# Kernel tuning notes

Hardware: AMD Instinct MI355X
Metric: run time of the kernel (lower is better)

Reference implementation:

```python
import jax, jax.numpy as jnp
import numpy as np

KD = 3  # kernel size per spatial dim
K = KD * KD * KD  # 27 taps


def conv3d(x, w, b, padding=1):
    # x: [B, C, D, H, W], w: [O, C, kd, kh, kw]
    pad = ((padding, padding),) * 3
    y = jax.lax.conv_general_dilated(
        x, w, window_strides=(1, 1, 1), padding=pad,
        dimension_numbers=('NCDHW', 'OIDHW', 'NCDHW'))
    return y + b[None, :, None, None, None]


def add_coords(x):
    # CoordConv: append 3 normalized coordinate channels in [-1, 1].
    B, C, D, H, W = x.shape
    z = jnp.linspace(-1.0, 1.0, D, dtype=x.dtype)[:, None, None]
    y = jnp.linspace(-1.0, 1.0, H, dtype=x.dtype)[None, :, None]
    xx = jnp.linspace(-1.0, 1.0, W, dtype=x.dtype)[None, None, :]
    coords = jnp.stack([
        jnp.broadcast_to(z, (D, H, W)),
        jnp.broadcast_to(y, (D, H, W)),
        jnp.broadcast_to(xx, (D, H, W)),
    ], axis=0)  # [3, D, H, W]
    coords = jnp.broadcast_to(coords[None], (B, 3, D, H, W))
    return jnp.concatenate([x, coords], axis=1)


def trilinear_sample(x, pos):
    # x: [B, C, D, H, W]; pos: [B, K, 3, D, H, W] absolute (z, y, x) sample coords.
    # Zero padding outside the volume. Returns [B, C, K, D, H, W].
    B, C, D, H, W = x.shape
    Kt = pos.shape[1]
    pz, py, px = pos[:, :, 0], pos[:, :, 1], pos[:, :, 2]  # [B, K, D, H, W]
    fz, fy, fx = jnp.floor(pz), jnp.floor(py), jnp.floor(px)
    x_flat = x.reshape(B, C, D * H * W)
    out = jnp.zeros((B, C, Kt, D, H, W), dtype=x.dtype)
    for cz in (0.0, 1.0):
        for cy in (0.0, 1.0):
            for cx in (0.0, 1.0):
                iz, iy, ix = fz + cz, fy + cy, fx + cx
                wgt = ((1.0 - jnp.abs(pz - iz)) *
                       (1.0 - jnp.abs(py - iy)) *
                       (1.0 - jnp.abs(px - ix)))
                valid = ((iz >= 0) & (iz < D) & (iy >= 0) & (iy < H)
                         & (ix >= 0) & (ix < W))
                izc = jnp.clip(iz, 0, D - 1).astype(jnp.int32)
                iyc = jnp.clip(iy, 0, H - 1).astype(jnp.int32)
                ixc = jnp.clip(ix, 0, W - 1).astype(jnp.int32)
                flat = ((izc * H + iyc) * W + ixc).reshape(B, -1)  # [B, K*DHW]
                vals = jax.vmap(lambda xf, idx: jnp.take(xf, idx, axis=1))(x_flat, flat)
                vals = vals.reshape(B, C, Kt, D, H, W)
                out = out + (wgt * valid.astype(x.dtype))[:, None] * vals
    return out


def modulated_deform_conv3d(x, offsets, alpha, w, b):
    # x: [B, Cin, D, H, W]; offsets: [B, 3K, D, H, W]; alpha: [B, K, D, H, W]
    # w: [O, Cin, 3, 3, 3]; stride 1, padding 1, dilation 1.
    B, Cin, D, H, W = x.shape
    off = offsets.reshape(B, K, 3, D, H, W)
    # Base sampling grid per tap: voxel position + kernel offset (pad=1 -> -1..1).
    dz = jnp.arange(D, dtype=x.dtype)[:, None, None]
    dy = jnp.arange(H, dtype=x.dtype)[None, :, None]
    dx = jnp.arange(W, dtype=x.dtype)[None, None, :]
    base = jnp.stack([
        jnp.broadcast_to(dz, (D, H, W)),
        jnp.broadcast_to(dy, (D, H, W)),
        jnp.broadcast_to(dx, (D, H, W)),
    ], axis=0)  # [3, D, H, W]
    kg = jnp.arange(KD, dtype=x.dtype) - 1.0  # [-1, 0, 1]
    kpos = jnp.stack(jnp.meshgrid(kg, kg, kg, indexing='ij'),
                     axis=-1).reshape(K, 3)  # [K, 3] in (kd, kh, kw) order
    pos = base[None, None] + kpos[None, :, :, None, None, None] + off  # [B,K,3,D,H,W]
    sampled = trilinear_sample(x, pos)  # [B, Cin, K, D, H, W]
    sampled = sampled * alpha[:, None]  # modulation
    wk = w.reshape(w.shape[0], Cin, K)
    out = jnp.einsum('bckv,ock->bov', sampled.reshape(B, Cin, K, D * H * W), wk)
    return out.reshape(B, -1, D, H, W) + b[None, :, None, None, None]


def setup_inputs() -> dict:
    key = jax.random.key(0)
    ks = jax.random.split(key, 4)
    B, Cin, Cout, D, H, W = 2, 64, 64, 8, 32, 32
    x = jax.random.normal(ks[0], (B, Cin, D, H, W), dtype=jnp.float32)
    # Small init on offset branch keeps sampling near the regular grid.
    w_off = jax.random.normal(ks[1], (108, Cin + 3, 3, 3, 3), jnp.float32) * 0.01
    b_off = jnp.zeros((108,), jnp.float32)
    w_dcn = jax.random.normal(ks[2], (Cout, Cin, 3, 3, 3), jnp.float32) * (1.0 / np.sqrt(Cin * 27))
    b_dcn = jnp.zeros((Cout,), jnp.float32)
    return {"x": x, "w_off": w_off, "b_off": b_off, "w_dcn": w_dcn, "b_dcn": b_dcn}


def reference(x, w_off, b_off, w_dcn, b_dcn):
    # CoordConv3d offset/mask prediction
    pred = conv3d(add_coords(x), w_off, b_off, padding=1)  # [B, 108, D, H, W]
    offsets, alpha = pred[:, :81], pred[:, 81:]
    alpha = jax.nn.sigmoid(alpha)  # [B, 27, D, H, W]
    return modulated_deform_conv3d(x, offsets, alpha, w_dcn, b_dcn)
```

## Files before the change

### kernel.cpp

```cpp
#include <hip/hip_runtime.h>

#define DHW  8192
#define COFF 108

typedef __attribute__((ext_vector_type(8))) short bf16x8;
typedef __attribute__((ext_vector_type(4))) float f32x4;
typedef __bf16 bfv2 __attribute__((ext_vector_type(2)));

__device__ inline unsigned short f2bf(float f) {
    unsigned u = __float_as_uint(f);
    u += 0x7fffu + ((u >> 16) & 1u);
    return (unsigned short)(u >> 16);
}
__device__ inline float bf2f(unsigned short h) {
    return __uint_as_float(((unsigned)h) << 16);
}

__device__ inline float dot2bf(unsigned a, unsigned b, float c) {
#if defined(__has_builtin) && __has_builtin(__builtin_amdgcn_fdot2_f32_bf16)
    return __builtin_amdgcn_fdot2_f32_bf16(__builtin_bit_cast(bfv2, a),
                                           __builtin_bit_cast(bfv2, b), c, false);
#else
    c += __uint_as_float(a << 16) * __uint_as_float(b << 16);
    c += __uint_as_float(a & 0xffff0000u) * __uint_as_float(b & 0xffff0000u);
    return c;
#endif
}

__global__ __launch_bounds__(256) void k_prep(
    const float* __restrict__ x, const float* __restrict__ w_off,
    const float* __restrict__ w_dcn,
    ushort* __restrict__ xt, ushort* __restrict__ pA1,
    ushort* __restrict__ pAc, ushort* __restrict__ pW)
{
    __shared__ ushort tile[16 * 66];
    const int bi = blockIdx.x;
    const int tid = threadIdx.x;
    if (bi < 1024) {
        const int b  = bi >> 9;
        const int f0 = (bi & 511) * 16;
        #pragma unroll
        for (int it = 0; it < 4; ++it) {
            int c = it * 16 + (tid >> 4), f = tid & 15;
            tile[f * 66 + c] = f2bf(x[((size_t)(b * 64 + c)) * DHW + f0 + f]);
        }
        __syncthreads();
        #pragma unroll
        for (int it = 0; it < 4; ++it) {
            int f = it * 4 + (tid >> 6), c = tid & 63;
            xt[((size_t)b * DHW + f0 + f) * 64 + c] = tile[f * 66 + c];
        }
    } else {
        int t0 = (bi - 1024) * 256 + tid;
        const int stride = 32 * 256;
        for (int i = t0; i < 27 * 2 * 7 * 512; i += stride) {
            int j = i & 7, l = (i >> 3) & 63, rest = i >> 9;
            int m = rest % 7, ch = (rest / 7) & 1, tap = rest / 14;
            int co = m * 16 + (l & 15);
            int ci = ch * 32 + (l >> 4) * 8 + j;
            pA1[i] = (co < COFF) ? f2bf(w_off[(co * 67 + ci) * 27 + tap]) : (ushort)0;
        }
        for (int i = t0; i < 3 * 7 * 512; i += stride) {
            int j = i & 7, l = (i >> 3) & 63, rest = i >> 9;
            int m = rest % 7, t = rest / 7;
            int co = m * 16 + (l & 15);
            int flatk = t * 32 + (l >> 4) * 8 + j;
            ushort v = 0;
            if (co < COFF && flatk < 81) {
                int cc = flatk / 27, tap = flatk % 27;
                v = f2bf(w_off[(co * 67 + 64 + cc) * 27 + tap]);
            }
            pAc[i] = v;
        }
        for (int i = t0; i < 27 * 2 * 4 * 512; i += stride) {
            int j = i & 7, l = (i >> 3) & 63;
            int m = (i >> 9) & 3, ch = (i >> 11) & 1, k = i >> 12;
            int o = m * 16 + (l & 15);
            int c = ch * 32 + (l >> 4) * 8 + j;
            pW[i] = f2bf(w_dcn[(o * 64 + c) * 27 + k]);
        }
    }
}

__global__ __launch_bounds__(512, 4) void k_fused(
    const ushort* __restrict__ xt, const ushort* __restrict__ pA1,
    const ushort* __restrict__ pAc, const ushort* __restrict__ pW,
    const float* __restrict__ b_off, const float* __restrict__ b_dcn,
    float* __restrict__ out)
{
    __shared__ __align__(16) char smem[64768];
    ushort* pred_lds = (ushort*)smem;
    char*   region   = smem + 6912;

    const int bi   = blockIdx.x;
    const int b    = bi >> 8;
    const int sp32 = bi & 255;
    const int d    = sp32 >> 5;
    const int h    = sp32 & 31;
    const int spg  = sp32 * 32;
    const int tid  = threadIdx.x;
    const int wv = tid >> 6, lane = tid & 63, q = lane >> 4, r16 = lane & 15;
    const ushort* __restrict__ xb = xt + (size_t)b * DHW * 64;

    f32x4 acc1[14] = {};
    for (int c = wv; c < 57; c += 8) {
        bf16x8 bf[2];
        const ushort* pa;
        if (c < 54) {
            int tap = c >> 1, ch = c & 1;
            int dz = tap / 9, rem9 = tap - dz * 9, dy = rem9 / 3, dx = rem9 - dy * 3;
            int zz = d + dz - 1, yy = h + dy - 1;
            int basepos = (zz << 10) + (yy << 5);
            bool okzy = ((unsigned)zz < 8u) & ((unsigned)yy < 32u);
            #pragma unroll
            for (int pt = 0; pt < 2; ++pt) {
                int xx = pt * 16 + r16 + dx - 1;
                bool ok = okzy & ((unsigned)xx < 32u);
                bf16x8 tv = {};
                if (ok) tv = *(const bf16x8*)(xb + (size_t)(basepos + xx) * 64
                                              + ch * 32 + q * 8);
                bf[pt] = tv;
            }
            pa = pA1 + (size_t)((tap * 2 + ch) * 7) * 512 + lane * 8;
        } else {
            int t = c - 54;
            #pragma unroll
            for (int pt = 0; pt < 2; ++pt) {
                bf16x8 bt;
                #pragma unroll
                for (int j = 0; j < 8; ++j) {
                    int flatk = t * 32 + q * 8 + j;
                    int cc = flatk / 27, tap = flatk % 27;
                    int dz = tap / 9, rem9 = tap - dz * 9, dy = rem9 / 3, dx = rem9 - dy * 3;
                    int zz = d + dz - 1, yy = h + dy - 1, xx = pt * 16 + r16 + dx - 1;
                    bool ok = (flatk < 81) & ((unsigned)zz < 8u) & ((unsigned)yy < 32u)
                              & ((unsigned)xx < 32u);
                    float val = 0.f;
                    if (ok)
                        val = (cc == 0) ? (-1.f + (2.f / 7.f) * (float)zz)
                            : (cc == 1) ? (-1.f + (2.f / 31.f) * (float)yy)
                                        : (-1.f + (2.f / 31.f) * (float)xx);
                    bt[j] = (short)f2bf(val);
                }
                bf[pt] = bt;
            }
            pa = pAc + (size_t)(t * 7) * 512 + lane * 8;
        }
        #pragma unroll
        for (int m = 0; m < 7; ++m) {
            bf16x8 af = *(const bf16x8*)(pa + m * 512);
            acc1[m * 2 + 0] = __builtin_amdgcn_mfma_f32_16x16x32_bf16(af, bf[0], acc1[m * 2 + 0], 0, 0, 0);
            acc1[m * 2 + 1] = __builtin_amdgcn_mfma_f32_16x16x32_bf16(af, bf[1], acc1[m * 2 + 1], 0, 0, 0);
        }
    }
    {
        uint2* red1 = (uint2*)region;
        #pragma unroll
        for (int i = 0; i < 14; ++i) {
            f32x4 s = acc1[i];
            uint2 pk2;
            pk2.x = (unsigned)f2bf(s[0]) | ((unsigned)f2bf(s[1]) << 16);
            pk2.y = (unsigned)f2bf(s[2]) | ((unsigned)f2bf(s[3]) << 16);
            red1[(wv * 14 + i) * 64 + lane] = pk2;
        }
        __syncthreads();
        for (int i = wv; i < 14; i += 8) {
            float s0 = 0.f, s1 = 0.f, s2 = 0.f, s3 = 0.f;
            #pragma unroll
            for (int sw = 0; sw < 8; ++sw) {
                uint2 v = red1[(sw * 14 + i) * 64 + lane];
                s0 += bf2f((unsigned short)(v.x & 0xffffu));
                s1 += bf2f((unsigned short)(v.x >> 16));
                s2 += bf2f((unsigned short)(v.y & 0xffffu));
                s3 += bf2f((unsigned short)(v.y >> 16));
            }
            int m = i >> 1, pt = i & 1;
            float sr[4] = {s0, s1, s2, s3};
            #pragma unroll
            for (int r = 0; r < 4; ++r) {
                int co = m * 16 + q * 4 + r;
                if (co < COFF)
                    pred_lds[co * 32 + pt * 16 + r16] = f2bf(sr[r] + b_off[co]);
            }
        }
        __syncthreads();
    }

    uint4* cwi = (uint4*)region;
    uint4* cww = (uint4*)(region + 27648);
    for (int kp = tid; kp < 27 * 32; kp += 512) {
        int k = kp >> 5, p = kp & 31;
        float offz = bf2f(pred_lds[(k * 3 + 0) * 32 + p]);
        float offy = bf2f(pred_lds[(k * 3 + 1) * 32 + p]);
        float offx = bf2f(pred_lds[(k * 3 + 2) * 32 + p]);
        float av   = bf2f(pred_lds[(81 + k) * 32 + p]);
        float alpha = 1.f / (1.f + __expf(-av));
        int kz = k / 9, rem = k - kz * 9, ky = rem / 3, kx = rem - ky * 3;
        float pz = (float)(d + kz - 1) + offz;
        float py = (float)(h + ky - 1) + offy;
        float px = (float)(p + kx - 1) + offx;
        float fz = floorf(pz), fy = floorf(py), fx = floorf(px);
        float tz = pz - fz, ty = py - fy, tx = px - fx;
        int iz0 = (int)fz, iy0 = (int)fy, ix0 = (int)fx;
        unsigned idxs[8]; float wgts[8];
        #pragma unroll
        for (int c8 = 0; c8 < 8; ++c8) {
            int czi = c8 >> 2, cyi = (c8 >> 1) & 1, cxi = c8 & 1;
            int iz = iz0 + czi, iy = iy0 + cyi, ix = ix0 + cxi;
            float wz = czi ? tz : 1.f - tz;
            float wy = cyi ? ty : 1.f - ty;
            float wx = cxi ? tx : 1.f - tx;
            bool ok = ((unsigned)iz < 8u) && ((unsigned)iy < 32u) && ((unsigned)ix < 32u);
            idxs[c8] = ok ? ((unsigned)((iz << 10) + (iy << 5) + ix) << 7) : 0u;
            wgts[c8] = ok ? wz * wy * wx * alpha : 0.f;
        }
        cwi[(k * 2 + 0) * 32 + p] = make_uint4(idxs[0], idxs[1], idxs[2], idxs[3]);
        cwi[(k * 2 + 1) * 32 + p] = make_uint4(idxs[4], idxs[5], idxs[6], idxs[7]);
        cww[k * 32 + p] = make_uint4(
            (unsigned)f2bf(wgts[0]) | ((unsigned)f2bf(wgts[1]) << 16),
            (unsigned)f2bf(wgts[2]) | ((unsigned)f2bf(wgts[3]) << 16),
            (unsigned)f2bf(wgts[4]) | ((unsigned)f2bf(wgts[5]) << 16),
            (unsigned)f2bf(wgts[6]) | ((unsigned)f2bf(wgts[7]) << 16));
    }
    __syncthreads();

    char* Sbuf = region + 41472;
    const int str = wv >> 2, pq = wv & 3;
    const int pr = lane >> 3, cg = lane & 7;
    const int p2 = pq * 8 + pr;
    const int m4 = wv & 3, ch = wv >> 2;
    const char* xbB = (const char*)xb + cg * 16;
    const unsigned swz_w = (unsigned)(str * 8192 + p2 * 128 + ((cg * 16) ^ ((p2 & 7) << 4)));
    unsigned swz_r[2];
    #pragma unroll
    for (int pt = 0; pt < 2; ++pt) {
        int p = pt * 16 + r16;
        swz_r[pt] = (unsigned)(p * 128 + ((ch * 64 + q * 16) ^ ((p & 7) << 4)));
    }

    f32x4 acc2[2] = {};
    for (int t = 0; t < 14; ++t) {
        const int ks0 = 2 * t + str;
        if (ks0 < 27) {
            uint4 wq = cww[ks0 * 32 + p2];
            uint4 i0 = cwi[(ks0 * 2 + 0) * 32 + p2];
            uint4 i1 = cwi[(ks0 * 2 + 1) * 32 + p2];
            unsigned iv[8] = {i0.x, i0.y, i0.z, i0.w, i1.x, i1.y, i1.z, i1.w};
            uint4 xv[8];
            #pragma unroll
            for (int c8 = 0; c8 < 8; ++c8)
                xv[c8] = *(const uint4*)(xbB + iv[c8]);
            unsigned wp[4] = {wq.x, wq.y, wq.z, wq.w};
            float sa[8] = {};
            #pragma unroll
            for (int cp = 0; cp < 4; ++cp) {
                unsigned ua[4] = {xv[cp * 2 + 0].x, xv[cp * 2 + 0].y, xv[cp * 2 + 0].z, xv[cp * 2 + 0].w};
                unsigned ub[4] = {xv[cp * 2 + 1].x, xv[cp * 2 + 1].y, xv[cp * 2 + 1].z, xv[cp * 2 + 1].w};
                #pragma unroll
                for (int dw = 0; dw < 4; ++dw) {
                    unsigned plo = __builtin_amdgcn_perm(ub[dw], ua[dw], 0x05040100u);
                    unsigned phi = __builtin_amdgcn_perm(ub[dw], ua[dw], 0x07060302u);
                    sa[dw * 2 + 0] = dot2bf(plo, wp[cp], sa[dw * 2 + 0]);
                    sa[dw * 2 + 1] = dot2bf(phi, wp[cp], sa[dw * 2 + 1]);
                }
            }
            uint4 pk;
            pk.x = (unsigned)f2bf(sa[0]) | ((unsigned)f2bf(sa[1]) << 16);
            pk.y = (unsigned)f2bf(sa[2]) | ((unsigned)f2bf(sa[3]) << 16);
            pk.z = (unsigned)f2bf(sa[4]) | ((unsigned)f2bf(sa[5]) << 16);
            pk.w = (unsigned)f2bf(sa[6]) | ((unsigned)f2bf(sa[7]) << 16);
            *(uint4*)(Sbuf + (t & 1) * 4096 + swz_w) = pk;
        }
        __syncthreads();
        #pragma unroll
        for (int ks = 0; ks < 2; ++ks) {
            int k = 2 * t + ks;
            if (k < 27) {
                bf16x8 af = *(const bf16x8*)(pW + (size_t)((k * 2 + ch) * 4 + m4) * 512 + lane * 8);
                #pragma unroll
                for (int pt = 0; pt < 2; ++pt) {
                    bf16x8 bv = *(const bf16x8*)(Sbuf + ks * 8192 + (t & 1) * 4096 + swz_r[pt]);
                    acc2[pt] = __builtin_amdgcn_mfma_f32_16x16x32_bf16(af, bv, acc2[pt], 0, 0, 0);
                }
            }
        }
    }

    __syncthreads();
    f32x4* red2 = (f32x4*)(region + 41472);
    if (wv >= 4) {
        red2[(m4 * 2 + 0) * 64 + lane] = acc2[0];
        red2[(m4 * 2 + 1) * 64 + lane] = acc2[1];
    }
    __syncthreads();
    if (wv < 4) {
        float* __restrict__ outb = out + (size_t)b * 64 * DHW + spg;
        #pragma unroll
        for (int pt = 0; pt < 2; ++pt) {
            f32x4 s = acc2[pt] + red2[(m4 * 2 + pt) * 64 + lane];
            #pragma unroll
            for (int r = 0; r < 4; ++r) {
                int o = m4 * 16 + q * 4 + r;
                outb[(size_t)o * DHW + pt * 16 + r16] = s[r] + b_dcn[o];
            }
        }
    }
}

extern "C" void kernel_launch(void* const* d_in, const int* in_sizes, int n_in,
                              void* d_out, int out_size, void* d_ws, size_t ws_size,
                              hipStream_t stream) {
    const float* x     = (const float*)d_in[0];
    const float* w_off = (const float*)d_in[1];
    const float* b_off = (const float*)d_in[2];
    const float* w_dcn = (const float*)d_in[3];
    const float* b_dcn = (const float*)d_in[4];
    float* out = (float*)d_out;

    ushort* xt  = (ushort*)d_ws;
    ushort* pA1 = (ushort*)((char*)d_ws + 2097152);
    ushort* pAc = (ushort*)((char*)d_ws + 2484224);
    ushort* pW  = (ushort*)((char*)d_ws + 2505728);

    k_prep <<<1056, 256, 0, stream>>>(x, w_off, w_dcn, xt, pA1, pAc, pW);
    k_fused<<<512, 512, 0, stream>>>(xt, pA1, pAc, pW, b_off, b_dcn, out);
}
```

Baseline: 65.34 us.

## Replace LDS staging and per-tap barriers with in-wave bpermute for deform GEMM

Each wave now gathers and interpolates its own slice of sampled values and moves them into MFMA B-fragment layout with ds_bpermute. This removes the double-buffered LDS staging buffer and the __syncthreads inside the 14-step tap loop. Waves split the work by point-half, channel-half and tap parity, and each wave runs 4 MFMAs per tap over all output rows. A final 8-way LDS reduction combines the partial sums. The trade-off is more weight-fragment loads per wave, a larger final reduction, and four bpermutes per tap.

```diff
diff --git a/kernel.cpp b/kernel.cpp
--- a/kernel.cpp
+++ b/kernel.cpp
@@ -88,7 +88,7 @@
     const float* __restrict__ b_off, const float* __restrict__ b_dcn,
     float* __restrict__ out)
 {
-    __shared__ __align__(16) char smem[64768];
+    __shared__ __align__(16) char smem[64256];
     ushort* pred_lds = (ushort*)smem;
     char*   region   = smem + 6912;
 
@@ -224,85 +224,69 @@
     }
     __syncthreads();
 
-    char* Sbuf = region + 41472;
-    const int str = wv >> 2, pq = wv & 3;
-    const int pr = lane >> 3, cg = lane & 7;
-    const int p2 = pq * 8 + pr;
-    const int m4 = wv & 3, ch = wv >> 2;
-    const char* xbB = (const char*)xb + cg * 16;
-    const unsigned swz_w = (unsigned)(str * 8192 + p2 * 128 + ((cg * 16) ^ ((p2 & 7) << 4)));
-    unsigned swz_r[2];
+    const int pt2 = wv & 1, ch2 = (wv >> 1) & 1, kh = wv >> 2;
+    const int pr = lane >> 2, cg = lane & 3;
+    const int p2 = pt2 * 16 + pr;
+    const char* xbB = (const char*)xb + ch2 * 64 + cg * 16;
+    const int baddr = (r16 * 4 + q) << 2;
+    f32x4 acc2[4] = {};
+    for (int k = kh; k < 27; k += 2) {
+        uint4 wq = cww[k * 32 + p2];
+        uint4 i0 = cwi[(k * 2 + 0) * 32 + p2];
+        uint4 i1 = cwi[(k * 2 + 1) * 32 + p2];
+        unsigned iv[8] = {i0.x, i0.y, i0.z, i0.w, i1.x, i1.y, i1.z, i1.w};
+        uint4 xv[8];
+        #pragma unroll
+        for (int c8 = 0; c8 < 8; ++c8)
+            xv[c8] = *(const uint4*)(xbB + iv[c8]);
+        unsigned wp[4] = {wq.x, wq.y, wq.z, wq.w};
+        float sa[8] = {};
+        #pragma unroll
+        for (int cp = 0; cp < 4; ++cp) {
+            unsigned ua[4] = {xv[cp * 2 + 0].x, xv[cp * 2 + 0].y, xv[cp * 2 + 0].z, xv[cp * 2 + 0].w};
+            unsigned ub[4] = {xv[cp * 2 + 1].x, xv[cp * 2 + 1].y, xv[cp * 2 + 1].z, xv[cp * 2 + 1].w};
+            #pragma unroll
+            for (int dw = 0; dw < 4; ++dw) {
+                unsigned plo = __builtin_amdgcn_perm(ub[dw], ua[dw], 0x05040100u);
+                unsigned phi = __builtin_amdgcn_perm(ub[dw], ua[dw], 0x07060302u);
+                sa[dw * 2 + 0] = dot2bf(plo, wp[cp], sa[dw * 2 + 0]);
+                sa[dw * 2 + 1] = dot2bf(phi, wp[cp], sa[dw * 2 + 1]);
+            }
+        }
+        unsigned pk0 = (unsigned)f2bf(sa[0]) | ((unsigned)f2bf(sa[1]) << 16);
+        unsigned pk1 = (unsigned)f2bf(sa[2]) | ((unsigned)f2bf(sa[3]) << 16);
+        unsigned pk2 = (unsigned)f2bf(sa[4]) | ((unsigned)f2bf(sa[5]) << 16);
+        unsigned pk3 = (unsigned)f2bf(sa[6]) | ((unsigned)f2bf(sa[7]) << 16);
+        uint4 bd;
+        bd.x = (unsigned)__builtin_amdgcn_ds_bpermute(baddr, (int)pk0);
+        bd.y = (unsigned)__builtin_amdgcn_ds_bpermute(baddr, (int)pk1);
+        bd.z = (unsigned)__builtin_amdgcn_ds_bpermute(baddr, (int)pk2);
+        bd.w = (unsigned)__builtin_amdgcn_ds_bpermute(baddr, (int)pk3);
+        bf16x8 bfrag = __builtin_bit_cast(bf16x8, bd);
+        const ushort* pwk = pW + (size_t)((k * 2 + ch2) * 4) * 512 + lane * 8;
+        #pragma unroll
+        for (int m = 0; m < 4; ++m)
+            acc2[m] = __builtin_amdgcn_mfma_f32_16x16x32_bf16(
+                *(const bf16x8*)(pwk + m * 512), bfrag, acc2[m], 0, 0, 0);
+    }
+
+    __syncthreads();
+    f32x4* red2 = (f32x4*)region;
     #pragma unroll
-    for (int pt = 0; pt < 2; ++pt) {
-        int p = pt * 16 + r16;
-        swz_r[pt] = (unsigned)(p * 128 + ((ch * 64 + q * 16) ^ ((p & 7) << 4)));
-    }
-
-    f32x4 acc2[2] = {};
-    for (int t = 0; t < 14; ++t) {
-        const int ks0 = 2 * t + str;
-        if (ks0 < 27) {
-            uint4 wq = cww[ks0 * 32 + p2];
-            uint4 i0 = cwi[(ks0 * 2 + 0) * 32 + p2];
-            uint4 i1 = cwi[(ks0 * 2 + 1) * 32 + p2];
-            unsigned iv[8] = {i0.x, i0.y, i0.z, i0.w, i1.x, i1.y, i1.z, i1.w};
-            uint4 xv[8];
-            #pragma unroll
-            for (int c8 = 0; c8 < 8; ++c8)
-                xv[c8] = *(const uint4*)(xbB + iv[c8]);
-            unsigned wp[4] = {wq.x, wq.y, wq.z, wq.w};
-            float sa[8] = {};
-            #pragma unroll
-            for (int cp = 0; cp < 4; ++cp) {
-                unsigned ua[4] = {xv[cp * 2 + 0].x, xv[cp * 2 + 0].y, xv[cp * 2 + 0].z, xv[cp * 2 + 0].w};
-                unsigned ub[4] = {xv[cp * 2 + 1].x, xv[cp * 2 + 1].y, xv[cp * 2 + 1].z, xv[cp * 2 + 1].w};
-                #pragma unroll
-                for (int dw = 0; dw < 4; ++dw) {
-                    unsigned plo = __builtin_amdgcn_perm(ub[dw], ua[dw], 0x05040100u);
-                    unsigned phi = __builtin_amdgcn_perm(ub[dw], ua[dw], 0x07060302u);
-                    sa[dw * 2 + 0] = dot2bf(plo, wp[cp], sa[dw * 2 + 0]);
-                    sa[dw * 2 + 1] = dot2bf(phi, wp[cp], sa[dw * 2 + 1]);
-                }
-            }
-            uint4 pk;
-            pk.x = (unsigned)f2bf(sa[0]) | ((unsigned)f2bf(sa[1]) << 16);
-            pk.y = (unsigned)f2bf(sa[2]) | ((unsigned)f2bf(sa[3]) << 16);
-            pk.z = (unsigned)f2bf(sa[4]) | ((unsigned)f2bf(sa[5]) << 16);
-            pk.w = (unsigned)f2bf(sa[6]) | ((unsigned)f2bf(sa[7]) << 16);
-            *(uint4*)(Sbuf + (t & 1) * 4096 + swz_w) = pk;
-        }
-        __syncthreads();
-        #pragma unroll
-        for (int ks = 0; ks < 2; ++ks) {
-            int k = 2 * t + ks;
-            if (k < 27) {
-                bf16x8 af = *(const bf16x8*)(pW + (size_t)((k * 2 + ch) * 4 + m4) * 512 + lane * 8);
-                #pragma unroll
-                for (int pt = 0; pt < 2; ++pt) {
-                    bf16x8 bv = *(const bf16x8*)(Sbuf + ks * 8192 + (t & 1) * 4096 + swz_r[pt]);
-                    acc2[pt] = __builtin_amdgcn_mfma_f32_16x16x32_bf16(af, bv, acc2[pt], 0, 0, 0);
-                }
-            }
-        }
-    }
-
+    for (int m = 0; m < 4; ++m)
+        red2[(wv * 4 + m) * 64 + lane] = acc2[m];
     __syncthreads();
-    f32x4* red2 = (f32x4*)(region + 41472);
-    if (wv >= 4) {
-        red2[(m4 * 2 + 0) * 64 + lane] = acc2[0];
-        red2[(m4 * 2 + 1) * 64 + lane] = acc2[1];
-    }
-    __syncthreads();
-    if (wv < 4) {
+    {
+        const int mo = wv >> 1, pto = wv & 1;
+        f32x4 s = red2[((pto + 0) * 4 + mo) * 64 + lane]
+                + red2[((pto + 2) * 4 + mo) * 64 + lane]
+                + red2[((pto + 4) * 4 + mo) * 64 + lane]
+                + red2[((pto + 6) * 4 + mo) * 64 + lane];
         float* __restrict__ outb = out + (size_t)b * 64 * DHW + spg;
         #pragma unroll
-        for (int pt = 0; pt < 2; ++pt) {
-            f32x4 s = acc2[pt] + red2[(m4 * 2 + pt) * 64 + lane];
-            #pragma unroll
-            for (int r = 0; r < 4; ++r) {
-                int o = m4 * 16 + q * 4 + r;
-                outb[(size_t)o * DHW + pt * 16 + r16] = s[r] + b_dcn[o];
-            }
+        for (int r = 0; r < 4; ++r) {
+            int o = mo * 16 + q * 4 + r;
+            outb[(size_t)o * DHW + pto * 16 + r16] = s[r] + b_dcn[o];
         }
     }
 }
```

Measured after the change: 64.42 us. Within noise of the previous version (-1.4%).
